# Performance work log

Hardware: AMD Instinct MI355X
Metric: run time of the kernel (lower is better)

## Reference

```python
import jax, jax.numpy as jnp
import numpy as np

N_NODES = 500_000
N_EDGES = 16_000_000


def setup_inputs() -> dict:
    key = jax.random.key(0)
    ks = jax.random.split(key, 10)
    x = jax.random.normal(ks[0], (N_NODES, 8), dtype=jnp.float32)
    edge_index = jax.random.randint(ks[1], (2, N_EDGES), 0, N_NODES, dtype=jnp.int64)
    W1_l = jax.random.normal(ks[2], (8, 32), dtype=jnp.float32) * 0.1
    W1_r = jax.random.normal(ks[3], (8, 32), dtype=jnp.float32) * 0.1
    b1 = jax.random.normal(ks[4], (32,), dtype=jnp.float32) * 0.1
    W2_l = jax.random.normal(ks[5], (32, 16), dtype=jnp.float32) * 0.1
    W2_r = jax.random.normal(ks[6], (32, 16), dtype=jnp.float32) * 0.1
    b2 = jax.random.normal(ks[7], (16,), dtype=jnp.float32) * 0.1
    W_out = jax.random.normal(ks[8], (16, 1), dtype=jnp.float32) * 0.1
    b_out = jax.random.normal(ks[9], (1,), dtype=jnp.float32) * 0.1
    return {"x": x, "edge_index": edge_index, "W1_l": W1_l, "W1_r": W1_r, "b1": b1,
            "W2_l": W2_l, "W2_r": W2_r, "b2": b2, "W_out": W_out, "b_out": b_out}


def _sage_conv(x, src, dst, deg_inv, W_l, W_r, b):
    # mean-aggregate neighbor features: gather x[src], scatter-add to dst, divide by degree
    agg = jax.ops.segment_sum(x[src], dst, num_segments=N_NODES)  # [N, d_in]
    mean_nb = agg * deg_inv[:, None]
    return mean_nb @ W_l + x @ W_r + b


def reference(x, edge_index, W1_l, W1_r, b1, W2_l, W2_r, b2, W_out, b_out):
    src, dst = edge_index[0], edge_index[1]
    # in-degree per target node (mean aggregation denominator), clamped at 1
    deg = jax.ops.segment_sum(jnp.ones((src.shape[0],), dtype=x.dtype), dst,
                              num_segments=N_NODES)
    deg_inv = 1.0 / jnp.maximum(deg, 1.0)
    h = jax.nn.relu(_sage_conv(x, src, dst, deg_inv, W1_l, W1_r, b1))
    # dropout(p=0.1) is identity at inference
    h = jax.nn.relu(_sage_conv(h, src, dst, deg_inv, W2_l, W2_r, b2))
    return jax.nn.sigmoid(h @ W_out + b_out)  # [N, 1]
```

## Files before the change

kernel.cpp:

```cpp
#include <hip/hip_runtime.h>
#include <hip/hip_fp16.h>
#include <math.h>

#define N_NODES 500000
#define N_EDGES 16000000

#define NBUCKET 2048
#define NPB 256
#define NSB 64
#define NSLICE 32
#define NB_USED 1954
#define BUCKET_CAP 9216

#define NCH_H 500
#define CHUNK_H 32000
#define NCH_A 1000
#define CHUNK_A 16000
#define T_A 4000
#define T_B 4000

#define OFF_TOT     0
#define OFF_BASE    8192
#define OFF_FCUR    16512
#define OFF_SBCUR   24704
#define OFF_AUXB    24960
#define OFF_ROW     25600
#define OFF_XH8     4025600
#define OFF_PAIRS   8025664
#define OFF_AUX     72025664
#define OFF_H1P8    72025664
#define OFF_S2      80025664
#define OFF_DEGQ    96025664

typedef float v2f __attribute__((ext_vector_type(2)));
typedef unsigned int v4u __attribute__((ext_vector_type(4)));

static __device__ inline float2 up2(unsigned int u) {
  __half2 h = *reinterpret_cast<__half2*>(&u);
  return __half22float2(h);
}
static __device__ inline unsigned int ph2(float a, float b) {
  __half2 h = __floats2half2_rn(a, b);
  return *reinterpret_cast<unsigned int*>(&h);
}
static __device__ inline unsigned int pk_fp8x4(float a, float b, float c, float d) {
  int u = __builtin_amdgcn_cvt_pk_fp8_f32(a, b, 0, false);
  u = __builtin_amdgcn_cvt_pk_fp8_f32(c, d, u, true);
  return (unsigned int)u;
}
static __device__ inline void acc8(float* a, uint2 g) {
  v2f f01 = __builtin_amdgcn_cvt_pk_f32_fp8((int)g.x, false);
  v2f f23 = __builtin_amdgcn_cvt_pk_f32_fp8((int)g.x, true);
  v2f f45 = __builtin_amdgcn_cvt_pk_f32_fp8((int)g.y, false);
  v2f f67 = __builtin_amdgcn_cvt_pk_f32_fp8((int)g.y, true);
  a[0] += f01.x; a[1] += f01.y; a[2] += f23.x; a[3] += f23.y;
  a[4] += f45.x; a[5] += f45.y; a[6] += f67.x; a[7] += f67.y;
}
static __device__ inline void acc16(float* a, uint4 g) {
  v2f f0 = __builtin_amdgcn_cvt_pk_f32_fp8((int)g.x, false);
  v2f f1 = __builtin_amdgcn_cvt_pk_f32_fp8((int)g.x, true);
  v2f f2 = __builtin_amdgcn_cvt_pk_f32_fp8((int)g.y, false);
  v2f f3 = __builtin_amdgcn_cvt_pk_f32_fp8((int)g.y, true);
  v2f f4 = __builtin_amdgcn_cvt_pk_f32_fp8((int)g.z, false);
  v2f f5 = __builtin_amdgcn_cvt_pk_f32_fp8((int)g.z, true);
  v2f f6 = __builtin_amdgcn_cvt_pk_f32_fp8((int)g.w, false);
  v2f f7 = __builtin_amdgcn_cvt_pk_f32_fp8((int)g.w, true);
  a[0] += f0.x;  a[1] += f0.y;  a[2] += f1.x;  a[3] += f1.y;
  a[4] += f2.x;  a[5] += f2.y;  a[6] += f3.x;  a[7] += f3.y;
  a[8] += f4.x;  a[9] += f4.y;  a[10] += f5.x; a[11] += f5.y;
  a[12] += f6.x; a[13] += f6.y; a[14] += f7.x; a[15] += f7.y;
}

__global__ __launch_bounds__(256) void k_xcast(const float* __restrict__ x,
                                               uint2* __restrict__ xh8) {
  int i = blockIdx.x * 256 + threadIdx.x;
  if (i >= N_NODES) return;
  const float4* xp = (const float4*)(x + (size_t)i * 8);
  float4 a = xp[0], b = xp[1];
  uint2 v;
  v.x = pk_fp8x4(a.x, a.y, a.z, a.w);
  v.y = pk_fp8x4(b.x, b.y, b.z, b.w);
  xh8[i] = v;
}

__global__ __launch_bounds__(256) void k_hist(const int* __restrict__ ei,
                                              int* __restrict__ tot) {
  __shared__ int hist[NBUCKET];
  int t = threadIdx.x;
  int c = blockIdx.x;
#pragma unroll
  for (int j = 0; j < NBUCKET / 256; j++) hist[t + j * 256] = 0;
  __syncthreads();
  int e0 = c * CHUNK_H;
  const int ng = CHUNK_H / 4;
  for (int g = t; g < ng; g += 256) {
    uint4 d4 = *(const uint4*)(ei + N_EDGES + e0 + g * 4);
    atomicAdd(&hist[d4.x >> 8], 1);
    atomicAdd(&hist[d4.y >> 8], 1);
    atomicAdd(&hist[d4.z >> 8], 1);
    atomicAdd(&hist[d4.w >> 8], 1);
  }
  __syncthreads();
#pragma unroll
  for (int j = 0; j < NBUCKET / 256; j++) {
    int b = t + j * 256;
    if (hist[b]) atomicAdd(&tot[b], hist[b]);
  }
}

__global__ __launch_bounds__(256) void k_scan(const int* __restrict__ tot,
                                              int* __restrict__ base,
                                              int* __restrict__ fineCur,
                                              int* __restrict__ sbCur,
                                              int* __restrict__ auxBase) {
  __shared__ int lds[256];
  int t = threadIdx.x;
  int loc[8];
  int s = 0;
#pragma unroll
  for (int j = 0; j < 8; j++) {
    loc[j] = s;
    s += tot[t * 8 + j];
  }
  lds[t] = s;
  __syncthreads();
  for (int off = 1; off < 256; off <<= 1) {
    int v = (t >= off) ? lds[t - off] : 0;
    __syncthreads();
    lds[t] += v;
    __syncthreads();
  }
  int eb = (t > 0) ? lds[t - 1] : 0;
#pragma unroll
  for (int j = 0; j < 8; j++) {
    int idx = t * 8 + j;
    int v = eb + loc[j];
    base[idx] = v;
    fineCur[idx] = v;
  }
  if (t == 255) base[NBUCKET] = lds[255];
  if (t < NSB) {
    int v = (t > 0) ? lds[t * 4 - 1] : 0;
    if (t >= 32) v -= lds[127];
    sbCur[t] = v;
    auxBase[t] = v;
  }
}

__global__ __launch_bounds__(256) void k_passA(const int* __restrict__ ei,
                                               int* __restrict__ sbCur,
                                               unsigned int* __restrict__ aux,
                                               int half) {
  __shared__ unsigned int ldsW[T_A];
  __shared__ unsigned char sid[T_A];
  __shared__ int hist[4 * 32];
  __shared__ int gbase[4 * 32];
  __shared__ int loff[32];
  __shared__ int lcur[32];
  __shared__ int tot_s;
  int t = threadIdx.x;
  int c = blockIdx.x;
  int e0 = c * CHUNK_A;
  int sb0 = half * 32;
  if (t < 128) hist[t] = 0;
  __syncthreads();
  {
    const int ng = CHUNK_A / 4;
    for (int g = t; g < ng; g += 256) {
      uint4 d4 = *(const uint4*)(ei + N_EDGES + e0 + g * 4);
      int tile = g / (T_A / 4);
      unsigned dd[4] = {d4.x, d4.y, d4.z, d4.w};
#pragma unroll
      for (int j = 0; j < 4; j++) {
        int sb = (int)(dd[j] >> 13);
        if ((sb >> 5) == half) atomicAdd(&hist[tile * 32 + (sb & 31)], 1);
      }
    }
  }
  __syncthreads();
  if (t < 32) {
    int h0 = hist[t], h1 = hist[32 + t], h2 = hist[64 + t], h3 = hist[96 + t];
    int g = atomicAdd(&sbCur[sb0 + t], h0 + h1 + h2 + h3);
    gbase[t] = g;
    gbase[32 + t] = g + h0;
    gbase[64 + t] = g + h0 + h1;
    gbase[96 + t] = g + h0 + h1 + h2;
  }
  __syncthreads();
  for (int ti = 0; ti < 4; ti++) {
    if (t == 0) {
      int r = 0;
      for (int s = 0; s < 32; s++) {
        loff[s] = r; lcur[s] = r; r += hist[ti * 32 + s];
      }
      tot_s = r;
    }
    __syncthreads();
    int tb = e0 + ti * T_A;
    const int ng = T_A / 4;
    for (int g = t; g < ng; g += 256) {
      uint4 s4 = *(const uint4*)(ei + tb + g * 4);
      uint4 d4 = *(const uint4*)(ei + N_EDGES + tb + g * 4);
      unsigned ss[4] = {s4.x, s4.y, s4.z, s4.w};
      unsigned dd[4] = {d4.x, d4.y, d4.z, d4.w};
#pragma unroll
      for (int j = 0; j < 4; j++) {
        int sb = (int)(dd[j] >> 13);
        if ((sb >> 5) == half) {
          int sl = sb & 31;
          int pos = atomicAdd(&lcur[sl], 1);
          ldsW[pos] = ss[j] | ((dd[j] & 8191u) << 19);
          sid[pos] = (unsigned char)sl;
        }
      }
    }
    __syncthreads();
    int tot2 = tot_s;
    for (int k = t; k < tot2; k += 256) {
      int s = sid[k];
      __builtin_nontemporal_store(ldsW[k], &aux[gbase[ti * 32 + s] + (k - loff[s])]);
    }
    __syncthreads();
  }
}

__global__ __launch_bounds__(256) void k_passB(const unsigned int* __restrict__ aux,
                                               const int* __restrict__ base,
                                               const int* __restrict__ auxBase,
                                               int* __restrict__ fineCur,
                                               unsigned int* __restrict__ pairs,
                                               int half) {
  __shared__ unsigned int ldsW[T_B];
  __shared__ unsigned char sid[T_B];
  __shared__ int hist[4 * 32];
  __shared__ int gbase[4 * 32];
  __shared__ int loff[32];
  __shared__ int lcur[32];
  __shared__ int tot_s;
  int t = threadIdx.x;
  int sbl = blockIdx.x / NSLICE;
  int sl = blockIdx.x % NSLICE;
  int sb = half * 32 + sbl;
  int aStart = auxBase[sb];
  int len = base[(sb + 1) << 5] - base[sb << 5];
  int per = (len + NSLICE - 1) / NSLICE;
  int lo = sl * per;
  int hi = lo + per;
  if (hi > len) hi = len;
  if (lo >= hi) return;
  int nt = (hi - lo + T_B - 1) / T_B;
  if (t < 128) hist[t] = 0;
  __syncthreads();
  for (int k = lo + t; k < hi; k += 256) {
    unsigned w = aux[aStart + k];
    int tile = (k - lo) / T_B;
    atomicAdd(&hist[tile * 32 + (int)(w >> 27)], 1);
  }
  __syncthreads();
  if (t < 32) {
    int h0 = hist[t], h1 = hist[32 + t], h2 = hist[64 + t], h3 = hist[96 + t];
    int g = atomicAdd(&fineCur[(sb << 5) + t], h0 + h1 + h2 + h3);
    gbase[t] = g;
    gbase[32 + t] = g + h0;
    gbase[64 + t] = g + h0 + h1;
    gbase[96 + t] = g + h0 + h1 + h2;
  }
  __syncthreads();
  for (int ti = 0; ti < nt; ti++) {
    if (t == 0) {
      int r = 0;
      for (int s = 0; s < 32; s++) {
        loff[s] = r; lcur[s] = r; r += hist[ti * 32 + s];
      }
      tot_s = r;
    }
    __syncthreads();
    int tl = lo + ti * T_B;
    int te = tl + T_B;
    if (te > hi) te = hi;
    for (int k = tl + t; k < te; k += 256) {
      unsigned w = aux[aStart + k];
      int s = (int)(w >> 27);
      int pos = atomicAdd(&lcur[s], 1);
      ldsW[pos] = w;
      sid[pos] = (unsigned char)s;
    }
    __syncthreads();
    int tot2 = tot_s;
    for (int k = t; k < tot2; k += 256) {
      int s = sid[k];
      __builtin_nontemporal_store(ldsW[k], &pairs[gbase[ti * 32 + s] + (k - loff[s])]);
    }
    __syncthreads();
  }
}

__global__ __launch_bounds__(256) void k_sort(unsigned int* __restrict__ pairs,
                                              const int* __restrict__ base,
                                              int* __restrict__ row,
                                              unsigned int* __restrict__ degq) {
  __shared__ unsigned int sp[BUCKET_CAP];
  __shared__ int hist[1024];
  __shared__ int cur[1024];
  __shared__ int lds[256];
  int t = threadIdx.x;
  int b = blockIdx.x;
  int e0 = base[b];
  int n = base[b + 1] - e0;
  if (n > BUCKET_CAP) n = BUCKET_CAP;
  for (int k = t; k < n; k += 256) sp[k] = pairs[e0 + k];
#pragma unroll
  for (int j = 0; j < 4; j++) hist[t + j * 256] = 0;
  __syncthreads();
  for (int k = t; k < n; k += 256) {
    unsigned int p = sp[k];
    int key = (int)(((p >> 19) & 255u) << 2) | (int)((p & 0x7FFFFu) >> 17);
    atomicAdd(&hist[key], 1);
  }
  __syncthreads();
  int h0 = hist[4 * t], h1 = hist[4 * t + 1], h2 = hist[4 * t + 2], h3 = hist[4 * t + 3];
  int s = h0 + h1 + h2 + h3;
  lds[t] = s;
  __syncthreads();
  for (int off = 1; off < 256; off <<= 1) {
    int v = (t >= off) ? lds[t - off] : 0;
    __syncthreads();
    lds[t] += v;
    __syncthreads();
  }
  int ebase = (t > 0) ? lds[t - 1] : 0;
  cur[4 * t] = e0 + ebase;
  cur[4 * t + 1] = e0 + ebase + h0;
  cur[4 * t + 2] = e0 + ebase + h0 + h1;
  cur[4 * t + 3] = e0 + ebase + h0 + h1 + h2;
  int i = (b << 8) + t;
  if (i < N_NODES) {
    row[i] = e0 + ebase;
    degq[i] = (unsigned)h0 | ((unsigned)h1 << 8) | ((unsigned)h2 << 16) |
              ((unsigned)h3 << 24);
  }
  __syncthreads();
  for (int k = t; k < n; k += 256) {
    unsigned int p = sp[k];
    int key = (int)(((p >> 19) & 255u) << 2) | (int)((p & 0x7FFFFu) >> 17);
    int pos = atomicAdd(&cur[key], 1);
    pairs[pos] = p & 0x7FFFFu;
  }
}

__global__ __launch_bounds__(256) void k_l1(
    const unsigned int* __restrict__ adj, const int* __restrict__ row,
    const unsigned int* __restrict__ degq, const uint2* __restrict__ xh8,
    const float* __restrict__ x,
    const float* __restrict__ W1l, const float* __restrict__ W1r,
    const float* __restrict__ b1,
    const float* __restrict__ W2l, const float* __restrict__ W2r,
    v4u* __restrict__ h1p8, v4u* __restrict__ s2) {
  __shared__ float sW1l[256], sW1r[256], sb1[32], sW2l[512], sW2r[512];
  int t = threadIdx.x;
  sW1l[t] = W1l[t];
  sW1r[t] = W1r[t];
  sW2l[t] = W2l[t];  sW2l[t + 256] = W2l[t + 256];
  sW2r[t] = W2r[t];  sW2r[t + 256] = W2r[t + 256];
  if (t < 32) sb1[t] = b1[t];
  __syncthreads();

  int i = blockIdx.x * 256 + t;
  bool act = i < N_NODES;
  int rs = act ? row[i] : 0;
  unsigned dq = act ? degq[i] : 0;
  int d = (int)((dq & 255u) + ((dq >> 8) & 255u) + ((dq >> 16) & 255u) + (dq >> 24));

  float acc[8] = {0, 0, 0, 0, 0, 0, 0, 0};
  int off = 0;
#pragma unroll
  for (int q = 0; q < 4; q++) {
    int len = (int)((dq >> (8 * q)) & 255u);
    int js = rs + off;
    int j = 0;
    for (; j + 4 <= len; j += 4) {
      int a0 = (int)__builtin_nontemporal_load(&adj[js + j + 0]);
      int a1 = (int)__builtin_nontemporal_load(&adj[js + j + 1]);
      int a2 = (int)__builtin_nontemporal_load(&adj[js + j + 2]);
      int a3 = (int)__builtin_nontemporal_load(&adj[js + j + 3]);
      uint2 g0 = xh8[a0], g1 = xh8[a1], g2 = xh8[a2], g3 = xh8[a3];
      acc8(acc, g0); acc8(acc, g1); acc8(acc, g2); acc8(acc, g3);
    }
    for (; j < len; j++) {
      uint2 g = xh8[(int)__builtin_nontemporal_load(&adj[js + j])];
      acc8(acc, g);
    }
    off += len;
    if (q < 3) __syncthreads();
  }

  if (!act) return;
  float dinv = 1.0f / fmaxf((float)d, 1.0f);
  float m[8];
#pragma unroll
  for (int f = 0; f < 8; f++) m[f] = acc[f] * dinv;
  const float4* xp = (const float4*)(x + (size_t)i * 8);
  float4 x0 = xp[0], x1 = xp[1];
  float xv[8] = {x0.x, x0.y, x0.z, x0.w, x1.x, x1.y, x1.z, x1.w};

  float h[32];
#pragma unroll
  for (int jj = 0; jj < 32; jj++) h[jj] = sb1[jj];
#pragma unroll
  for (int k = 0; k < 8; k++) {
#pragma unroll
    for (int jj = 0; jj < 32; jj++) {
      h[jj] = fmaf(m[k], sW1l[k * 32 + jj], h[jj]);
      h[jj] = fmaf(xv[k], sW1r[k * 32 + jj], h[jj]);
    }
  }
#pragma unroll
  for (int jj = 0; jj < 32; jj++) h[jj] = fmaxf(h[jj], 0.0f);

  float p[16], s[16];
#pragma unroll
  for (int jj = 0; jj < 16; jj++) { p[jj] = 0.0f; s[jj] = 0.0f; }
#pragma unroll
  for (int k = 0; k < 32; k++) {
#pragma unroll
    for (int jj = 0; jj < 16; jj++) {
      p[jj] = fmaf(h[k], sW2l[k * 16 + jj], p[jj]);
      s[jj] = fmaf(h[k], sW2r[k * 16 + jj], s[jj]);
    }
  }
  v4u hv;
  hv.x = pk_fp8x4(p[0], p[1], p[2], p[3]);
  hv.y = pk_fp8x4(p[4], p[5], p[6], p[7]);
  hv.z = pk_fp8x4(p[8], p[9], p[10], p[11]);
  hv.w = pk_fp8x4(p[12], p[13], p[14], p[15]);
  __builtin_nontemporal_store(hv, &h1p8[i]);
  v4u slo, shi;
  slo.x = ph2(s[0], s[1]);   slo.y = ph2(s[2], s[3]);
  slo.z = ph2(s[4], s[5]);   slo.w = ph2(s[6], s[7]);
  shi.x = ph2(s[8], s[9]);   shi.y = ph2(s[10], s[11]);
  shi.z = ph2(s[12], s[13]); shi.w = ph2(s[14], s[15]);
  __builtin_nontemporal_store(slo, &s2[(size_t)i * 2]);
  __builtin_nontemporal_store(shi, &s2[(size_t)i * 2 + 1]);
}

__global__ __launch_bounds__(256) void k_l2(
    const unsigned int* __restrict__ adj, const int* __restrict__ row,
    const unsigned int* __restrict__ degq, const uint4* __restrict__ h1p8,
    const v4u* __restrict__ s2, const float* __restrict__ b2,
    const float* __restrict__ Wout, const float* __restrict__ bout,
    float* __restrict__ out) {
  __shared__ float sb2[16], sWo[16], sbo;
  int t = threadIdx.x;
  if (t < 16) { sb2[t] = b2[t]; sWo[t] = Wout[t]; }
  if (t == 0) sbo = bout[0];
  __syncthreads();

  int i = blockIdx.x * 256 + t;
  bool act = i < N_NODES;
  int rs = act ? row[i] : 0;
  unsigned dq = act ? degq[i] : 0;
  int d = (int)((dq & 255u) + ((dq >> 8) & 255u) + ((dq >> 16) & 255u) + (dq >> 24));

  float acc[16];
#pragma unroll
  for (int jj = 0; jj < 16; jj++) acc[jj] = 0.0f;
  int off = 0;
#pragma unroll
  for (int q = 0; q < 4; q++) {
    int len = (int)((dq >> (8 * q)) & 255u);
    int js = rs + off;
    int j = 0;
    for (; j + 4 <= len; j += 4) {
      int a0 = (int)__builtin_nontemporal_load(&adj[js + j + 0]);
      int a1 = (int)__builtin_nontemporal_load(&adj[js + j + 1]);
      int a2 = (int)__builtin_nontemporal_load(&adj[js + j + 2]);
      int a3 = (int)__builtin_nontemporal_load(&adj[js + j + 3]);
      uint4 g0 = h1p8[a0], g1 = h1p8[a1], g2 = h1p8[a2], g3 = h1p8[a3];
      acc16(acc, g0); acc16(acc, g1); acc16(acc, g2); acc16(acc, g3);
    }
    for (; j < len; j++) {
      uint4 g = h1p8[(int)__builtin_nontemporal_load(&adj[js + j])];
      acc16(acc, g);
    }
    off += len;
    if (q < 3) __syncthreads();
  }

  if (!act) return;
  float dinv = 1.0f / fmaxf((float)d, 1.0f);
  v4u q0 = __builtin_nontemporal_load(&s2[(size_t)i * 2]);
  v4u q1 = __builtin_nontemporal_load(&s2[(size_t)i * 2 + 1]);
  float2 s0 = up2(q0.x), s1 = up2(q0.y), s2v = up2(q0.z), s3 = up2(q0.w);
  float2 s4 = up2(q1.x), s5 = up2(q1.y), s6 = up2(q1.z), s7 = up2(q1.w);
  float sv[16] = {s0.x, s0.y, s1.x, s1.y, s2v.x, s2v.y, s3.x, s3.y,
                  s4.x, s4.y, s5.x, s5.y, s6.x, s6.y, s7.x, s7.y};
  float o = sbo;
#pragma unroll
  for (int c = 0; c < 16; c++) {
    float h2 = fmaxf(acc[c] * dinv + sv[c] + sb2[c], 0.0f);
    o = fmaf(h2, sWo[c], o);
  }
  out[i] = 1.0f / (1.0f + expf(-o));
}

extern "C" void kernel_launch(void* const* d_in, const int* in_sizes, int n_in,
                              void* d_out, int out_size, void* d_ws, size_t ws_size,
                              hipStream_t stream) {
  const float* x    = (const float*)d_in[0];
  const int*   ei   = (const int*)d_in[1];
  const float* W1l  = (const float*)d_in[2];
  const float* W1r  = (const float*)d_in[3];
  const float* b1   = (const float*)d_in[4];
  const float* W2l  = (const float*)d_in[5];
  const float* W2r  = (const float*)d_in[6];
  const float* b2   = (const float*)d_in[7];
  const float* Wout = (const float*)d_in[8];
  const float* bout = (const float*)d_in[9];
  float* out = (float*)d_out;

  char* ws = (char*)d_ws;
  int* tot     = (int*)(ws + OFF_TOT);
  int* base    = (int*)(ws + OFF_BASE);
  int* fineCur = (int*)(ws + OFF_FCUR);
  int* sbCur   = (int*)(ws + OFF_SBCUR);
  int* auxBase = (int*)(ws + OFF_AUXB);
  int* row     = (int*)(ws + OFF_ROW);
  uint2* xh8   = (uint2*)(ws + OFF_XH8);
  unsigned int* pairs = (unsigned int*)(ws + OFF_PAIRS);
  unsigned int* aux   = (unsigned int*)(ws + OFF_AUX);
  v4u* h1p8    = (v4u*)(ws + OFF_H1P8);
  v4u* s2      = (v4u*)(ws + OFF_S2);
  unsigned int* degq = (unsigned int*)(ws + OFF_DEGQ);

  (void)hipMemsetAsync(tot, 0, NBUCKET * sizeof(int), stream);

  k_xcast<<<NB_USED, 256, 0, stream>>>(x, xh8);
  k_hist<<<NCH_H, 256, 0, stream>>>(ei, tot);
  k_scan<<<1, 256, 0, stream>>>(tot, base, fineCur, sbCur, auxBase);
  k_passA<<<NCH_A, 256, 0, stream>>>(ei, sbCur, aux, 0);
  k_passB<<<32 * NSLICE, 256, 0, stream>>>(aux, base, auxBase, fineCur, pairs, 0);
  k_passA<<<NCH_A, 256, 0, stream>>>(ei, sbCur, aux, 1);
  k_passB<<<32 * NSLICE, 256, 0, stream>>>(aux, base, auxBase, fineCur, pairs, 1);
  k_sort<<<NBUCKET, 256, 0, stream>>>(pairs, base, row, degq);
  k_l1<<<NB_USED, 256, 0, stream>>>(pairs, row, degq, xh8, x, W1l, W1r, b1,
                                    W2l, W2r, h1p8, s2);
  k_l2<<<NB_USED, 256, 0, stream>>>(pairs, row, degq, (const uint4*)h1p8, s2,
                                    b2, Wout, bout, out);
}
```

Baseline: 859.5 us.

## Drop per-bucket CSR sort; aggregate edges via LDS float atomics per 256-node bucket

Removes the k_sort kernel that built per-node CSR rows and packed degrees. Layer kernels now stream each bucket's edge list in order and scatter-add the decoded fp8 features into shared-memory accumulators with LDS atomics, counting degree the same way. Layer 2 also buckets edges into four source-range queues in LDS so gathers from h1p8 are grouped by source region, with an overflow fallback. This saves a full read-sort-write pass over the edges but adds many LDS float atomics per edge, and float summation order is no longer deterministic.

New measurement: 2.556 ms. 197% more time.

```diff
diff --git a/kernel.cpp b/kernel.cpp
--- a/kernel.cpp
+++ b/kernel.cpp
@@ -6,11 +6,9 @@
 #define N_EDGES 16000000
 
 #define NBUCKET 2048
-#define NPB 256
 #define NSB 64
 #define NSLICE 32
 #define NB_USED 1954
-#define BUCKET_CAP 9216
 
 #define NCH_H 500
 #define CHUNK_H 32000
@@ -18,19 +16,18 @@
 #define CHUNK_A 16000
 #define T_A 4000
 #define T_B 4000
+#define CAPQ 2112
 
 #define OFF_TOT     0
 #define OFF_BASE    8192
 #define OFF_FCUR    16512
 #define OFF_SBCUR   24704
 #define OFF_AUXB    24960
-#define OFF_ROW     25600
 #define OFF_XH8     4025600
 #define OFF_PAIRS   8025664
 #define OFF_AUX     72025664
 #define OFF_H1P8    72025664
 #define OFF_S2      80025664
-#define OFF_DEGQ    96025664
 
 typedef float v2f __attribute__((ext_vector_type(2)));
 typedef unsigned int v4u __attribute__((ext_vector_type(4)));
@@ -47,28 +44,6 @@
   int u = __builtin_amdgcn_cvt_pk_fp8_f32(a, b, 0, false);
   u = __builtin_amdgcn_cvt_pk_fp8_f32(c, d, u, true);
   return (unsigned int)u;
-}
-static __device__ inline void acc8(float* a, uint2 g) {
-  v2f f01 = __builtin_amdgcn_cvt_pk_f32_fp8((int)g.x, false);
-  v2f f23 = __builtin_amdgcn_cvt_pk_f32_fp8((int)g.x, true);
-  v2f f45 = __builtin_amdgcn_cvt_pk_f32_fp8((int)g.y, false);
-  v2f f67 = __builtin_amdgcn_cvt_pk_f32_fp8((int)g.y, true);
-  a[0] += f01.x; a[1] += f01.y; a[2] += f23.x; a[3] += f23.y;
-  a[4] += f45.x; a[5] += f45.y; a[6] += f67.x; a[7] += f67.y;
-}
-static __device__ inline void acc16(float* a, uint4 g) {
-  v2f f0 = __builtin_amdgcn_cvt_pk_f32_fp8((int)g.x, false);
-  v2f f1 = __builtin_amdgcn_cvt_pk_f32_fp8((int)g.x, true);
-  v2f f2 = __builtin_amdgcn_cvt_pk_f32_fp8((int)g.y, false);
-  v2f f3 = __builtin_amdgcn_cvt_pk_f32_fp8((int)g.y, true);
-  v2f f4 = __builtin_amdgcn_cvt_pk_f32_fp8((int)g.z, false);
-  v2f f5 = __builtin_amdgcn_cvt_pk_f32_fp8((int)g.z, true);
-  v2f f6 = __builtin_amdgcn_cvt_pk_f32_fp8((int)g.w, false);
-  v2f f7 = __builtin_amdgcn_cvt_pk_f32_fp8((int)g.w, true);
-  a[0] += f0.x;  a[1] += f0.y;  a[2] += f1.x;  a[3] += f1.y;
-  a[4] += f2.x;  a[5] += f2.y;  a[6] += f3.x;  a[7] += f3.y;
-  a[8] += f4.x;  a[9] += f4.y;  a[10] += f5.x; a[11] += f5.y;
-  a[12] += f6.x; a[13] += f6.y; a[14] += f7.x; a[15] += f7.y;
 }
 
 __global__ __launch_bounds__(256) void k_xcast(const float* __restrict__ x,
@@ -169,7 +144,7 @@
     for (int g = t; g < ng; g += 256) {
       uint4 d4 = *(const uint4*)(ei + N_EDGES + e0 + g * 4);
       int tile = g / (T_A / 4);
-      unsigned dd[4] = {d4.x, d4.y, d4.z, d4.w};
+      unsigned int dd[4] = {d4.x, d4.y, d4.z, d4.w};
 #pragma unroll
       for (int j = 0; j < 4; j++) {
         int sb = (int)(dd[j] >> 13);
@@ -201,8 +176,8 @@
     for (int g = t; g < ng; g += 256) {
       uint4 s4 = *(const uint4*)(ei + tb + g * 4);
       uint4 d4 = *(const uint4*)(ei + N_EDGES + tb + g * 4);
-      unsigned ss[4] = {s4.x, s4.y, s4.z, s4.w};
-      unsigned dd[4] = {d4.x, d4.y, d4.z, d4.w};
+      unsigned int ss[4] = {s4.x, s4.y, s4.z, s4.w};
+      unsigned int dd[4] = {d4.x, d4.y, d4.z, d4.w};
 #pragma unroll
       for (int j = 0; j < 4; j++) {
         int sb = (int)(dd[j] >> 13);
@@ -252,7 +227,7 @@
   if (t < 128) hist[t] = 0;
   __syncthreads();
   for (int k = lo + t; k < hi; k += 256) {
-    unsigned w = aux[aStart + k];
+    unsigned int w = aux[aStart + k];
     int tile = (k - lo) / T_B;
     atomicAdd(&hist[tile * 32 + (int)(w >> 27)], 1);
   }
@@ -279,7 +254,7 @@
     int te = tl + T_B;
     if (te > hi) te = hi;
     for (int k = tl + t; k < te; k += 256) {
-      unsigned w = aux[aStart + k];
+      unsigned int w = aux[aStart + k];
       int s = (int)(w >> 27);
       int pos = atomicAdd(&lcur[s], 1);
       ldsW[pos] = w;
@@ -295,67 +270,15 @@
   }
 }
 
-__global__ __launch_bounds__(256) void k_sort(unsigned int* __restrict__ pairs,
-                                              const int* __restrict__ base,
-                                              int* __restrict__ row,
-                                              unsigned int* __restrict__ degq) {
-  __shared__ unsigned int sp[BUCKET_CAP];
-  __shared__ int hist[1024];
-  __shared__ int cur[1024];
-  __shared__ int lds[256];
-  int t = threadIdx.x;
-  int b = blockIdx.x;
-  int e0 = base[b];
-  int n = base[b + 1] - e0;
-  if (n > BUCKET_CAP) n = BUCKET_CAP;
-  for (int k = t; k < n; k += 256) sp[k] = pairs[e0 + k];
-#pragma unroll
-  for (int j = 0; j < 4; j++) hist[t + j * 256] = 0;
-  __syncthreads();
-  for (int k = t; k < n; k += 256) {
-    unsigned int p = sp[k];
-    int key = (int)(((p >> 19) & 255u) << 2) | (int)((p & 0x7FFFFu) >> 17);
-    atomicAdd(&hist[key], 1);
-  }
-  __syncthreads();
-  int h0 = hist[4 * t], h1 = hist[4 * t + 1], h2 = hist[4 * t + 2], h3 = hist[4 * t + 3];
-  int s = h0 + h1 + h2 + h3;
-  lds[t] = s;
-  __syncthreads();
-  for (int off = 1; off < 256; off <<= 1) {
-    int v = (t >= off) ? lds[t - off] : 0;
-    __syncthreads();
-    lds[t] += v;
-    __syncthreads();
-  }
-  int ebase = (t > 0) ? lds[t - 1] : 0;
-  cur[4 * t] = e0 + ebase;
-  cur[4 * t + 1] = e0 + ebase + h0;
-  cur[4 * t + 2] = e0 + ebase + h0 + h1;
-  cur[4 * t + 3] = e0 + ebase + h0 + h1 + h2;
-  int i = (b << 8) + t;
-  if (i < N_NODES) {
-    row[i] = e0 + ebase;
-    degq[i] = (unsigned)h0 | ((unsigned)h1 << 8) | ((unsigned)h2 << 16) |
-              ((unsigned)h3 << 24);
-  }
-  __syncthreads();
-  for (int k = t; k < n; k += 256) {
-    unsigned int p = sp[k];
-    int key = (int)(((p >> 19) & 255u) << 2) | (int)((p & 0x7FFFFu) >> 17);
-    int pos = atomicAdd(&cur[key], 1);
-    pairs[pos] = p & 0x7FFFFu;
-  }
-}
-
 __global__ __launch_bounds__(256) void k_l1(
-    const unsigned int* __restrict__ adj, const int* __restrict__ row,
-    const unsigned int* __restrict__ degq, const uint2* __restrict__ xh8,
-    const float* __restrict__ x,
+    const unsigned int* __restrict__ pairs, const int* __restrict__ base,
+    const uint2* __restrict__ xh8, const float* __restrict__ x,
     const float* __restrict__ W1l, const float* __restrict__ W1r,
     const float* __restrict__ b1,
     const float* __restrict__ W2l, const float* __restrict__ W2r,
     v4u* __restrict__ h1p8, v4u* __restrict__ s2) {
+  __shared__ float acc[8][256];
+  __shared__ int deg[256];
   __shared__ float sW1l[256], sW1r[256], sb1[32], sW2l[512], sW2r[512];
   int t = threadIdx.x;
   sW1l[t] = W1l[t];
@@ -363,42 +286,48 @@
   sW2l[t] = W2l[t];  sW2l[t + 256] = W2l[t + 256];
   sW2r[t] = W2r[t];  sW2r[t + 256] = W2r[t + 256];
   if (t < 32) sb1[t] = b1[t];
-  __syncthreads();
-
-  int i = blockIdx.x * 256 + t;
-  bool act = i < N_NODES;
-  int rs = act ? row[i] : 0;
-  unsigned dq = act ? degq[i] : 0;
-  int d = (int)((dq & 255u) + ((dq >> 8) & 255u) + ((dq >> 16) & 255u) + (dq >> 24));
-
-  float acc[8] = {0, 0, 0, 0, 0, 0, 0, 0};
-  int off = 0;
-#pragma unroll
-  for (int q = 0; q < 4; q++) {
-    int len = (int)((dq >> (8 * q)) & 255u);
-    int js = rs + off;
-    int j = 0;
-    for (; j + 4 <= len; j += 4) {
-      int a0 = (int)__builtin_nontemporal_load(&adj[js + j + 0]);
-      int a1 = (int)__builtin_nontemporal_load(&adj[js + j + 1]);
-      int a2 = (int)__builtin_nontemporal_load(&adj[js + j + 2]);
-      int a3 = (int)__builtin_nontemporal_load(&adj[js + j + 3]);
-      uint2 g0 = xh8[a0], g1 = xh8[a1], g2 = xh8[a2], g3 = xh8[a3];
-      acc8(acc, g0); acc8(acc, g1); acc8(acc, g2); acc8(acc, g3);
-    }
-    for (; j < len; j++) {
-      uint2 g = xh8[(int)__builtin_nontemporal_load(&adj[js + j])];
-      acc8(acc, g);
-    }
-    off += len;
-    if (q < 3) __syncthreads();
-  }
-
-  if (!act) return;
-  float dinv = 1.0f / fmaxf((float)d, 1.0f);
+#pragma unroll
+  for (int f = 0; f < 8; f++) acc[f][t] = 0.0f;
+  deg[t] = 0;
+  __syncthreads();
+
+  auto scat = [&](unsigned int w, uint2 g) {
+    int ld = (int)((w >> 19) & 255u);
+    v2f f01 = __builtin_amdgcn_cvt_pk_f32_fp8((int)g.x, false);
+    v2f f23 = __builtin_amdgcn_cvt_pk_f32_fp8((int)g.x, true);
+    v2f f45 = __builtin_amdgcn_cvt_pk_f32_fp8((int)g.y, false);
+    v2f f67 = __builtin_amdgcn_cvt_pk_f32_fp8((int)g.y, true);
+    atomicAdd(&acc[0][ld], f01.x); atomicAdd(&acc[1][ld], f01.y);
+    atomicAdd(&acc[2][ld], f23.x); atomicAdd(&acc[3][ld], f23.y);
+    atomicAdd(&acc[4][ld], f45.x); atomicAdd(&acc[5][ld], f45.y);
+    atomicAdd(&acc[6][ld], f67.x); atomicAdd(&acc[7][ld], f67.y);
+    atomicAdd(&deg[ld], 1);
+  };
+
+  int b = blockIdx.x;
+  int e0 = base[b], e1 = base[b + 1];
+  int kk = e0 + t;
+  for (; kk + 768 < e1; kk += 1024) {
+    unsigned int w0 = __builtin_nontemporal_load(&pairs[kk]);
+    unsigned int w1 = __builtin_nontemporal_load(&pairs[kk + 256]);
+    unsigned int w2 = __builtin_nontemporal_load(&pairs[kk + 512]);
+    unsigned int w3 = __builtin_nontemporal_load(&pairs[kk + 768]);
+    uint2 g0 = xh8[w0 & 0x7FFFFu], g1 = xh8[w1 & 0x7FFFFu];
+    uint2 g2 = xh8[w2 & 0x7FFFFu], g3 = xh8[w3 & 0x7FFFFu];
+    scat(w0, g0); scat(w1, g1); scat(w2, g2); scat(w3, g3);
+  }
+  for (; kk < e1; kk += 256) {
+    unsigned int w = __builtin_nontemporal_load(&pairs[kk]);
+    scat(w, xh8[w & 0x7FFFFu]);
+  }
+  __syncthreads();
+
+  int i = b * 256 + t;
+  if (i >= N_NODES) return;
+  float dinv = 1.0f / fmaxf((float)deg[t], 1.0f);
   float m[8];
 #pragma unroll
-  for (int f = 0; f < 8; f++) m[f] = acc[f] * dinv;
+  for (int f = 0; f < 8; f++) m[f] = acc[f][t] * dinv;
   const float4* xp = (const float4*)(x + (size_t)i * 8);
   float4 x0 = xp[0], x1 = xp[1];
   float xv[8] = {x0.x, x0.y, x0.z, x0.w, x1.x, x1.y, x1.z, x1.w};
@@ -444,50 +373,94 @@
 }
 
 __global__ __launch_bounds__(256) void k_l2(
-    const unsigned int* __restrict__ adj, const int* __restrict__ row,
-    const unsigned int* __restrict__ degq, const uint4* __restrict__ h1p8,
-    const v4u* __restrict__ s2, const float* __restrict__ b2,
-    const float* __restrict__ Wout, const float* __restrict__ bout,
-    float* __restrict__ out) {
+    const unsigned int* __restrict__ pairs, const int* __restrict__ base,
+    const uint4* __restrict__ h1p8, const v4u* __restrict__ s2,
+    const float* __restrict__ b2, const float* __restrict__ Wout,
+    const float* __restrict__ bout, float* __restrict__ out) {
+  __shared__ unsigned int Q[4][CAPQ];
+  __shared__ float acc[16][256];
+  __shared__ int deg[256];
+  __shared__ int qcur[4];
   __shared__ float sb2[16], sWo[16], sbo;
   int t = threadIdx.x;
+#pragma unroll
+  for (int f = 0; f < 16; f++) acc[f][t] = 0.0f;
+  deg[t] = 0;
+  if (t < 4) qcur[t] = 0;
   if (t < 16) { sb2[t] = b2[t]; sWo[t] = Wout[t]; }
   if (t == 0) sbo = bout[0];
   __syncthreads();
 
-  int i = blockIdx.x * 256 + t;
-  bool act = i < N_NODES;
-  int rs = act ? row[i] : 0;
-  unsigned dq = act ? degq[i] : 0;
-  int d = (int)((dq & 255u) + ((dq >> 8) & 255u) + ((dq >> 16) & 255u) + (dq >> 24));
-
-  float acc[16];
-#pragma unroll
-  for (int jj = 0; jj < 16; jj++) acc[jj] = 0.0f;
-  int off = 0;
-#pragma unroll
-  for (int q = 0; q < 4; q++) {
-    int len = (int)((dq >> (8 * q)) & 255u);
-    int js = rs + off;
-    int j = 0;
-    for (; j + 4 <= len; j += 4) {
-      int a0 = (int)__builtin_nontemporal_load(&adj[js + j + 0]);
-      int a1 = (int)__builtin_nontemporal_load(&adj[js + j + 1]);
-      int a2 = (int)__builtin_nontemporal_load(&adj[js + j + 2]);
-      int a3 = (int)__builtin_nontemporal_load(&adj[js + j + 3]);
-      uint4 g0 = h1p8[a0], g1 = h1p8[a1], g2 = h1p8[a2], g3 = h1p8[a3];
-      acc16(acc, g0); acc16(acc, g1); acc16(acc, g2); acc16(acc, g3);
-    }
-    for (; j < len; j++) {
-      uint4 g = h1p8[(int)__builtin_nontemporal_load(&adj[js + j])];
-      acc16(acc, g);
-    }
-    off += len;
-    if (q < 3) __syncthreads();
-  }
-
-  if (!act) return;
-  float dinv = 1.0f / fmaxf((float)d, 1.0f);
+  auto scat = [&](unsigned int w, uint4 g) {
+    int ld = (int)((w >> 19) & 255u);
+    v2f f0 = __builtin_amdgcn_cvt_pk_f32_fp8((int)g.x, false);
+    v2f f1 = __builtin_amdgcn_cvt_pk_f32_fp8((int)g.x, true);
+    v2f f2 = __builtin_amdgcn_cvt_pk_f32_fp8((int)g.y, false);
+    v2f f3 = __builtin_amdgcn_cvt_pk_f32_fp8((int)g.y, true);
+    v2f f4 = __builtin_amdgcn_cvt_pk_f32_fp8((int)g.z, false);
+    v2f f5 = __builtin_amdgcn_cvt_pk_f32_fp8((int)g.z, true);
+    v2f f6 = __builtin_amdgcn_cvt_pk_f32_fp8((int)g.w, false);
+    v2f f7 = __builtin_amdgcn_cvt_pk_f32_fp8((int)g.w, true);
+    atomicAdd(&acc[0][ld], f0.x);   atomicAdd(&acc[1][ld], f0.y);
+    atomicAdd(&acc[2][ld], f1.x);   atomicAdd(&acc[3][ld], f1.y);
+    atomicAdd(&acc[4][ld], f2.x);   atomicAdd(&acc[5][ld], f2.y);
+    atomicAdd(&acc[6][ld], f3.x);   atomicAdd(&acc[7][ld], f3.y);
+    atomicAdd(&acc[8][ld], f4.x);   atomicAdd(&acc[9][ld], f4.y);
+    atomicAdd(&acc[10][ld], f5.x);  atomicAdd(&acc[11][ld], f5.y);
+    atomicAdd(&acc[12][ld], f6.x);  atomicAdd(&acc[13][ld], f6.y);
+    atomicAdd(&acc[14][ld], f7.x);  atomicAdd(&acc[15][ld], f7.y);
+    atomicAdd(&deg[ld], 1);
+  };
+
+  int b = blockIdx.x;
+  int e0 = base[b], e1 = base[b + 1];
+  int lane = t & 63;
+  unsigned long long ltm = (1ull << lane) - 1ull;
+  int n = e1 - e0;
+  int nit = (n + 255) >> 8;
+  for (int it = 0; it < nit; it++) {
+    int k = e0 + (it << 8) + t;
+    bool v = k < e1;
+    unsigned int w = v ? __builtin_nontemporal_load(&pairs[k]) : 0u;
+    int q = v ? (int)(((unsigned long long)(w & 0x7FFFFu) * 34360ull) >> 32) : 4;
+#pragma unroll
+    for (int qq = 0; qq < 4; qq++) {
+      unsigned long long m = __ballot(q == qq);
+      if (!m) continue;
+      int leader = __ffsll((unsigned long long)m) - 1;
+      int bs = 0;
+      if (lane == leader) bs = atomicAdd(&qcur[qq], (int)__popcll(m));
+      bs = __shfl(bs, leader);
+      if (q == qq) {
+        int pos = bs + (int)__popcll(m & ltm);
+        if (pos < CAPQ) Q[qq][pos] = w;
+        else scat(w, h1p8[w & 0x7FFFFu]);
+      }
+    }
+  }
+  __syncthreads();
+#pragma unroll
+  for (int qq = 0; qq < 4; qq++) {
+    int cnt = qcur[qq];
+    if (cnt > CAPQ) cnt = CAPQ;
+    int k = t;
+    for (; k + 768 < cnt; k += 1024) {
+      unsigned int w0 = Q[qq][k], w1 = Q[qq][k + 256];
+      unsigned int w2 = Q[qq][k + 512], w3 = Q[qq][k + 768];
+      uint4 g0 = h1p8[w0 & 0x7FFFFu], g1 = h1p8[w1 & 0x7FFFFu];
+      uint4 g2 = h1p8[w2 & 0x7FFFFu], g3 = h1p8[w3 & 0x7FFFFu];
+      scat(w0, g0); scat(w1, g1); scat(w2, g2); scat(w3, g3);
+    }
+    for (; k < cnt; k += 256) {
+      unsigned int w = Q[qq][k];
+      scat(w, h1p8[w & 0x7FFFFu]);
+    }
+    __syncthreads();
+  }
+
+  int i = b * 256 + t;
+  if (i >= N_NODES) return;
+  float dinv = 1.0f / fmaxf((float)deg[t], 1.0f);
   v4u q0 = __builtin_nontemporal_load(&s2[(size_t)i * 2]);
   v4u q1 = __builtin_nontemporal_load(&s2[(size_t)i * 2 + 1]);
   float2 s0 = up2(q0.x), s1 = up2(q0.y), s2v = up2(q0.z), s3 = up2(q0.w);
@@ -497,7 +470,7 @@
   float o = sbo;
 #pragma unroll
   for (int c = 0; c < 16; c++) {
-    float h2 = fmaxf(acc[c] * dinv + sv[c] + sb2[c], 0.0f);
+    float h2 = fmaxf(acc[c][t] * dinv + sv[c] + sb2[c], 0.0f);
     o = fmaf(h2, sWo[c], o);
   }
   out[i] = 1.0f / (1.0f + expf(-o));
@@ -524,13 +497,11 @@
   int* fineCur = (int*)(ws + OFF_FCUR);
   int* sbCur   = (int*)(ws + OFF_SBCUR);
   int* auxBase = (int*)(ws + OFF_AUXB);
-  int* row     = (int*)(ws + OFF_ROW);
   uint2* xh8   = (uint2*)(ws + OFF_XH8);
   unsigned int* pairs = (unsigned int*)(ws + OFF_PAIRS);
   unsigned int* aux   = (unsigned int*)(ws + OFF_AUX);
   v4u* h1p8    = (v4u*)(ws + OFF_H1P8);
   v4u* s2      = (v4u*)(ws + OFF_S2);
-  unsigned int* degq = (unsigned int*)(ws + OFF_DEGQ);
 
   (void)hipMemsetAsync(tot, 0, NBUCKET * sizeof(int), stream);
 
@@ -541,9 +512,8 @@
   k_passB<<<32 * NSLICE, 256, 0, stream>>>(aux, base, auxBase, fineCur, pairs, 0);
   k_passA<<<NCH_A, 256, 0, stream>>>(ei, sbCur, aux, 1);
   k_passB<<<32 * NSLICE, 256, 0, stream>>>(aux, base, auxBase, fineCur, pairs, 1);
-  k_sort<<<NBUCKET, 256, 0, stream>>>(pairs, base, row, degq);
-  k_l1<<<NB_USED, 256, 0, stream>>>(pairs, row, degq, xh8, x, W1l, W1r, b1,
+  k_l1<<<NB_USED, 256, 0, stream>>>(pairs, base, xh8, x, W1l, W1r, b1,
                                     W2l, W2r, h1p8, s2);
-  k_l2<<<NB_USED, 256, 0, stream>>>(pairs, row, degq, (const uint4*)h1p8, s2,
+  k_l2<<<NB_USED, 256, 0, stream>>>(pairs, base, (const uint4*)h1p8, s2,
                                     b2, Wout, bout, out);
 }
```

## Aggregate LDS atomics per wavefront with ballots and drop quarter-phase barriers

Applied to the files above, without the earlier changes.

Replaces per-element LDS atomicAdd in the histogram and scatter phases of passA and passB with wavefront-level aggregation. For each of 32 sub-buckets the code does a ballot, one leader atomic carrying the popcount, and a shuffle plus prefix popcount to assign positions. This cuts LDS atomic contention at the cost of a 32-iteration ballot loop per element. In the layer-1 gather kernel the four degree-quarter segments with __syncthreads between them are merged into one loop, so each thread walks its whole neighbour list and inactive threads exit early.

Result: slower. 2.176 ms (+153.1%).

```diff
diff --git a/kernel.cpp b/kernel.cpp
--- a/kernel.cpp
+++ b/kernel.cpp
@@ -6,7 +6,6 @@
 #define N_EDGES 16000000
 
 #define NBUCKET 2048
-#define NPB 256
 #define NSB 64
 #define NSLICE 32
 #define NB_USED 1954
@@ -17,6 +16,7 @@
 #define NCH_A 1000
 #define CHUNK_A 16000
 #define T_A 4000
+#define GPT 1000
 #define T_B 4000
 
 #define OFF_TOT     0
@@ -159,21 +159,27 @@
   __shared__ int lcur[32];
   __shared__ int tot_s;
   int t = threadIdx.x;
+  int lane = t & 63;
+  unsigned long long ltm = (1ull << lane) - 1ull;
   int c = blockIdx.x;
   int e0 = c * CHUNK_A;
   int sb0 = half * 32;
   if (t < 128) hist[t] = 0;
   __syncthreads();
-  {
-    const int ng = CHUNK_A / 4;
-    for (int g = t; g < ng; g += 256) {
+  for (int ti = 0; ti < 4; ti++) {
+    for (int g = ti * GPT + t; g < (ti + 1) * GPT; g += 256) {
       uint4 d4 = *(const uint4*)(ei + N_EDGES + e0 + g * 4);
-      int tile = g / (T_A / 4);
-      unsigned dd[4] = {d4.x, d4.y, d4.z, d4.w};
+      unsigned int dd[4] = {d4.x, d4.y, d4.z, d4.w};
 #pragma unroll
       for (int j = 0; j < 4; j++) {
         int sb = (int)(dd[j] >> 13);
-        if ((sb >> 5) == half) atomicAdd(&hist[tile * 32 + (sb & 31)], 1);
+        int sl = ((sb >> 5) == half) ? (sb & 31) : -1;
+        for (int s = 0; s < 32; s++) {
+          unsigned long long m = __ballot(sl == s);
+          if (!m) continue;
+          if (lane == __ffsll((unsigned long long)m) - 1)
+            atomicAdd(&hist[ti * 32 + s], (int)__popcll(m));
+        }
       }
     }
   }
@@ -197,21 +203,27 @@
     }
     __syncthreads();
     int tb = e0 + ti * T_A;
-    const int ng = T_A / 4;
-    for (int g = t; g < ng; g += 256) {
+    for (int g = t; g < GPT; g += 256) {
       uint4 s4 = *(const uint4*)(ei + tb + g * 4);
       uint4 d4 = *(const uint4*)(ei + N_EDGES + tb + g * 4);
-      unsigned ss[4] = {s4.x, s4.y, s4.z, s4.w};
-      unsigned dd[4] = {d4.x, d4.y, d4.z, d4.w};
+      unsigned int ss[4] = {s4.x, s4.y, s4.z, s4.w};
+      unsigned int dd[4] = {d4.x, d4.y, d4.z, d4.w};
 #pragma unroll
       for (int j = 0; j < 4; j++) {
         int sb = (int)(dd[j] >> 13);
-        if ((sb >> 5) == half) {
-          int sl = sb & 31;
-          int pos = atomicAdd(&lcur[sl], 1);
-          ldsW[pos] = ss[j] | ((dd[j] & 8191u) << 19);
-          sid[pos] = (unsigned char)sl;
+        int sl = ((sb >> 5) == half) ? (sb & 31) : -1;
+        unsigned int w = ss[j] | ((dd[j] & 8191u) << 19);
+        int pos = -1;
+        for (int s = 0; s < 32; s++) {
+          unsigned long long m = __ballot(sl == s);
+          if (!m) continue;
+          int leader = __ffsll((unsigned long long)m) - 1;
+          int bs = 0;
+          if (lane == leader) bs = atomicAdd(&lcur[s], (int)__popcll(m));
+          bs = __shfl(bs, leader);
+          if (sl == s) pos = bs + (int)__popcll(m & ltm);
         }
+        if (pos >= 0) { ldsW[pos] = w; sid[pos] = (unsigned char)sl; }
       }
     }
     __syncthreads();
@@ -238,23 +250,34 @@
   __shared__ int lcur[32];
   __shared__ int tot_s;
   int t = threadIdx.x;
+  int lane = t & 63;
+  unsigned long long ltm = (1ull << lane) - 1ull;
   int sbl = blockIdx.x / NSLICE;
-  int sl = blockIdx.x % NSLICE;
+  int sl2 = blockIdx.x % NSLICE;
   int sb = half * 32 + sbl;
   int aStart = auxBase[sb];
   int len = base[(sb + 1) << 5] - base[sb << 5];
   int per = (len + NSLICE - 1) / NSLICE;
-  int lo = sl * per;
+  int lo = sl2 * per;
   int hi = lo + per;
   if (hi > len) hi = len;
   if (lo >= hi) return;
   int nt = (hi - lo + T_B - 1) / T_B;
   if (t < 128) hist[t] = 0;
   __syncthreads();
-  for (int k = lo + t; k < hi; k += 256) {
-    unsigned w = aux[aStart + k];
-    int tile = (k - lo) / T_B;
-    atomicAdd(&hist[tile * 32 + (int)(w >> 27)], 1);
+  for (int ti = 0; ti < nt; ti++) {
+    int tl = lo + ti * T_B;
+    int te = tl + T_B; if (te > hi) te = hi;
+    for (int k = tl + t; k < te; k += 256) {
+      unsigned int w = aux[aStart + k];
+      int s0 = (int)(w >> 27);
+      for (int s = 0; s < 32; s++) {
+        unsigned long long m = __ballot(s0 == s);
+        if (!m) continue;
+        if (lane == __ffsll((unsigned long long)m) - 1)
+          atomicAdd(&hist[ti * 32 + s], (int)__popcll(m));
+      }
+    }
   }
   __syncthreads();
   if (t < 32) {
@@ -276,14 +299,21 @@
     }
     __syncthreads();
     int tl = lo + ti * T_B;
-    int te = tl + T_B;
-    if (te > hi) te = hi;
+    int te = tl + T_B; if (te > hi) te = hi;
     for (int k = tl + t; k < te; k += 256) {
-      unsigned w = aux[aStart + k];
-      int s = (int)(w >> 27);
-      int pos = atomicAdd(&lcur[s], 1);
-      ldsW[pos] = w;
-      sid[pos] = (unsigned char)s;
+      unsigned int w = aux[aStart + k];
+      int s0 = (int)(w >> 27);
+      int pos = -1;
+      for (int s = 0; s < 32; s++) {
+        unsigned long long m = __ballot(s0 == s);
+        if (!m) continue;
+        int leader = __ffsll((unsigned long long)m) - 1;
+        int bs = 0;
+        if (lane == leader) bs = atomicAdd(&lcur[s], (int)__popcll(m));
+        bs = __shfl(bs, leader);
+        if (s0 == s) pos = bs + (int)__popcll(m & ltm);
+      }
+      if (pos >= 0) { ldsW[pos] = w; sid[pos] = (unsigned char)s0; }
     }
     __syncthreads();
     int tot2 = tot_s;
@@ -366,35 +396,26 @@
   __syncthreads();
 
   int i = blockIdx.x * 256 + t;
-  bool act = i < N_NODES;
-  int rs = act ? row[i] : 0;
-  unsigned dq = act ? degq[i] : 0;
+  if (i >= N_NODES) return;
+  int rs = row[i];
+  unsigned dq = degq[i];
   int d = (int)((dq & 255u) + ((dq >> 8) & 255u) + ((dq >> 16) & 255u) + (dq >> 24));
 
   float acc[8] = {0, 0, 0, 0, 0, 0, 0, 0};
-  int off = 0;
-#pragma unroll
-  for (int q = 0; q < 4; q++) {
-    int len = (int)((dq >> (8 * q)) & 255u);
-    int js = rs + off;
-    int j = 0;
-    for (; j + 4 <= len; j += 4) {
-      int a0 = (int)__builtin_nontemporal_load(&adj[js + j + 0]);
-      int a1 = (int)__builtin_nontemporal_load(&adj[js + j + 1]);
-      int a2 = (int)__builtin_nontemporal_load(&adj[js + j + 2]);
-      int a3 = (int)__builtin_nontemporal_load(&adj[js + j + 3]);
-      uint2 g0 = xh8[a0], g1 = xh8[a1], g2 = xh8[a2], g3 = xh8[a3];
-      acc8(acc, g0); acc8(acc, g1); acc8(acc, g2); acc8(acc, g3);
-    }
-    for (; j < len; j++) {
-      uint2 g = xh8[(int)__builtin_nontemporal_load(&adj[js + j])];
-      acc8(acc, g);
-    }
-    off += len;
-    if (q < 3) __syncthreads();
-  }
-
-  if (!act) return;
+  int j = 0;
+  for (; j + 4 <= d; j += 4) {
+    int a0 = (int)__builtin_nontemporal_load(&adj[rs + j + 0]);
+    int a1 = (int)__builtin_nontemporal_load(&adj[rs + j + 1]);
+    int a2 = (int)__builtin_nontemporal_load(&adj[rs + j + 2]);
+    int a3 = (int)__builtin_nontemporal_load(&adj[rs + j + 3]);
+    uint2 g0 = xh8[a0], g1 = xh8[a1], g2 = xh8[a2], g3 = xh8[a3];
+    acc8(acc, g0); acc8(acc, g1); acc8(acc, g2); acc8(acc, g3);
+  }
+  for (; j < d; j++) {
+    uint2 g = xh8[(int)__builtin_nontemporal_load(&adj[rs + j])];
+    acc8(acc, g);
+  }
+
   float dinv = 1.0f / fmaxf((float)d, 1.0f);
   float m[8];
 #pragma unroll
```
